# Optimization experiments

Hardware: AMD Instinct MI355X
Metric: run time of the kernel (lower is better)

## Reference

```python
import jax, jax.numpy as jnp
import numpy as np

_PADE_B = np.array([6.476475253248e+16, 3.238237626624e+16, 7771770303897600.0,
                    1187353796428800.0, 129060195264000.0, 10559470521600.0,
                    670442572800.0, 33522128640.0, 1323241920.0, 40840800.0,
                    960960.0, 16380.0, 182.0, 1.0])
_MAXNORM = 5.371920351148152
_MAX_SQUARINGS = 6  # randn 3x3 has Fro norm ~3 < maxnorm; 6 steps is ample headroom


def _expm(A):
    """Batched scaling-and-squaring Pade-13 matrix exponential. A: [N, d, d]."""
    b = _PADE_B.astype(A.dtype)
    d = A.shape[-1]
    ident = jnp.eye(d, dtype=A.dtype)
    fro = jnp.sqrt(jnp.sum(A * A, axis=(1, 2), keepdims=True))  # [N,1,1]
    n_sq = jnp.maximum(0.0, jnp.ceil(jnp.log2(fro / _MAXNORM)))
    Ascaled = A / (2.0 ** n_sq)
    n_sq_i = n_sq.reshape(-1).astype(jnp.int32)  # [N]

    A2 = Ascaled @ Ascaled
    A4 = A2 @ A2
    A6 = A4 @ A2
    U = Ascaled @ (A6 @ (b[13] * A6 + b[11] * A4 + b[9] * A2)
                   + b[7] * A6 + b[5] * A4 + b[3] * A2 + b[1] * ident)
    V = (A6 @ (b[12] * A6 + b[10] * A4 + b[8] * A2)
         + b[6] * A6 + b[4] * A4 + b[2] * A2 + b[0] * ident)
    P = U + V
    Q = -U + V
    R = jnp.linalg.solve(Q, P)  # torch.solve(P, Q): Q X = P

    def body(k, R):
        R2 = R @ R
        return jnp.where((k < n_sq_i)[:, None, None], R2, R)

    return jax.lax.fori_loop(0, _MAX_SQUARINGS, body, R, unroll=True)


def setup_inputs() -> dict:
    key = jax.random.key(0)
    k1, k2, k3 = jax.random.split(key, 3)
    bs, n, d = 65536, 24, 3
    return {
        "mean": jax.random.normal(k1, (bs, n, d), dtype=jnp.float32),
        "var": jax.random.normal(k2, (bs, n, d, d), dtype=jnp.float32),
        "gt": jax.random.normal(k3, (bs, n, d), dtype=jnp.float32),
    }


def reference(mean, var, gt):
    bs, n, d = mean.shape
    A = var.reshape(bs * n, d, d)
    E = _expm(A)                               # [bs*n, d, d]
    delta = (gt - mean).reshape(bs * n, d)     # [bs*n, d]
    quad = jnp.einsum('ni,nij,nj->n', delta, E, delta)
    dets = jnp.linalg.det(A)
    per = 0.5 * (quad + dets) / n              # [bs*n]
    loss = per.reshape(bs, n).sum(axis=1)      # [bs]
    return loss.mean()
```

## Files before the change

### kernel.cpp

```cpp
#include <hip/hip_runtime.h>

#define TPB 256

#define B0c  6.476475253248e+16f
#define B1c  3.238237626624e+16f
#define B2c  7.7717703038976e+15f
#define B3c  1.1873537964288e+15f
#define B4c  1.29060195264e+14f
#define B5c  1.05594705216e+13f
#define B6c  6.704425728e+11f
#define B7c  3.352212864e+10f
#define B8c  1.32324192e+9f
#define B9c  4.08408e+7f
#define B10c 9.6096e+5f
#define B11c 1.638e+4f
#define B12c 182.0f
#define B13c 1.0f

__device__ __forceinline__ float expm_loss_one(
    float a0, float a1, float a2, float a3, float a4, float a5,
    float a6, float a7, float a8, float d0, float d1, float d2) {
  const float detA = a0 * (a4 * a8 - a5 * a7)
                   - a1 * (a3 * a8 - a5 * a6)
                   + a2 * (a3 * a7 - a4 * a6);
  const float trA = a0 + a4 + a8;
  const float trA2 = fmaf(a0, a0, fmaf(a4, a4, a8 * a8))
                   + 2.0f * (fmaf(a1, a3, fmaf(a2, a6, a5 * a7)));
  float fro2 = fmaf(a0, a0, fmaf(a1, a1, a2 * a2));
  fro2 = fmaf(a3, a3, fmaf(a4, a4, fmaf(a5, a5, fro2)));
  fro2 = fmaf(a6, a6, fmaf(a7, a7, fmaf(a8, a8, fro2)));
  const float u0 = fmaf(a0, d0, fmaf(a1, d1, a2 * d2));
  const float u1 = fmaf(a3, d0, fmaf(a4, d1, a5 * d2));
  const float u2 = fmaf(a6, d0, fmaf(a7, d1, a8 * d2));
  const float v0 = fmaf(a0, d0, fmaf(a3, d1, a6 * d2));
  const float v1 = fmaf(a1, d0, fmaf(a4, d1, a7 * d2));
  const float v2 = fmaf(a2, d0, fmaf(a5, d1, a8 * d2));
  const float dAd  = fmaf(d0, u0, fmaf(d1, u1, d2 * u2));
  const float dA2d = fmaf(v0, u0, fmaf(v1, u1, v2 * u2));
  const float dd   = fmaf(d0, d0, fmaf(d1, d1, d2 * d2));

  const float nsqf = fmaxf(0.0f, ceilf(fmaf(0.5f, __log2f(fro2), -2.4253625f)));
  int nsq = (int)nsqf;
  nsq = nsq > 6 ? 6 : nsq;
  const float scl = exp2f(-nsqf);
  const float scl2 = scl * scl;

  const float t = scl * trA;
  const float trB2 = scl2 * trA2;
  const float m = 0.5f * fmaf(t, t, -trB2);
  const float dch = detA * scl2 * scl;

  const float x4p = fmaf(t, t, -m), x4q = fmaf(-t, m, dch), x4r = t * dch;
  const float x5p = fmaf(x4p, t, x4q), x5q = fmaf(-x4p, m, x4r), x5r = x4p * dch;
  const float x6p = fmaf(x5p, t, x5q), x6q = fmaf(-x5p, m, x5r), x6r = x5p * dch;

  const float w1p = fmaf(B11c, x4p, x6p) + B9c;
  const float w1q = fmaf(B11c, x4q, x6q);
  const float w1r = fmaf(B11c, x4r, x6r);
  const float s4a = x6p * w1p;
  const float s3a = fmaf(x6p, w1q, x6q * w1p);
  const float gp = fmaf(s4a, x4p, fmaf(s3a, t,   fmaf(x6p, w1r, fmaf(x6r, w1p, x6q * w1q))));
  const float gq = fmaf(s4a, x4q, fmaf(-s3a, m,  fmaf(x6q, w1r, x6r * w1q)));
  const float gr = fmaf(s4a, x4r, fmaf(s3a, dch, x6r * w1r));
  const float uep = fmaf(B7c, x6p, fmaf(B5c, x4p, gp)) + B3c;
  const float ueq = fmaf(B7c, x6q, fmaf(B5c, x4q, gq));
  const float uer = fmaf(B7c, x6r, fmaf(B5c, x4r, gr)) + B1c;
  const float up = fmaf(uep, t, ueq);
  const float uq = fmaf(-uep, m, uer);
  const float ur = uep * dch;

  const float w2p = fmaf(B12c, x6p, fmaf(B10c, x4p, B8c));
  const float w2q = fmaf(B12c, x6q, B10c * x4q);
  const float w2r = fmaf(B12c, x6r, B10c * x4r);
  const float s4b = x6p * w2p;
  const float s3b = fmaf(x6p, w2q, x6q * w2p);
  const float hp = fmaf(s4b, x4p, fmaf(s3b, t,   fmaf(x6p, w2r, fmaf(x6r, w2p, x6q * w2q))));
  const float hq = fmaf(s4b, x4q, fmaf(-s3b, m,  fmaf(x6q, w2r, x6r * w2q)));
  const float hr = fmaf(s4b, x4r, fmaf(s3b, dch, x6r * w2r));
  const float vp = fmaf(B6c, x6p, fmaf(B4c, x4p, hp)) + B2c;
  const float vq = fmaf(B6c, x6q, fmaf(B4c, x4q, hq));
  const float vr = fmaf(B6c, x6r, fmaf(B4c, x4r, hr)) + B0c;

  const float s = 1.0f / B0c;
  const float pp = (vp + up) * s, pq = (vq + uq) * s, pr = (vr + ur) * s;
  const float qp = (vp - up) * s, qq = (vq - uq) * s, qr = (vr - ur) * s;

  const float qpp = qp * qp, qpq2 = 2.0f * qp * qq;
  const float a2t = fmaf(qpp, x4p, fmaf(qpq2, t,   fmaf(2.0f * qp, qr, qq * qq)));
  const float b2t = fmaf(qpp, x4q, fmaf(-qpq2, m,  2.0f * qq * qr));
  const float c2t = fmaf(qpp, x4r, fmaf(qpq2, dch, qr * qr));
  const float tQ = fmaf(qp, trB2, fmaf(qq, t, 3.0f * qr));
  const float trQ2 = fmaf(a2t, trB2, fmaf(b2t, t, 3.0f * c2t));
  const float mQ = 0.5f * fmaf(tQ, tQ, -trQ2);
  const float detQ =
      qp * (fmaf(qp, fmaf(qp, dch * dch, fmaf(qq, m * dch, qr * fmaf(m, m, -2.0f * t * dch))),
                 fmaf(qq, fmaf(qq, t * dch, qr * fmaf(t, m, -3.0f * dch)),
                      qr * qr * fmaf(t, t, -2.0f * m))))
    + qq * fmaf(qq, fmaf(qq, dch, qr * m), qr * qr * t)
    + qr * qr * qr;
  float inv = __builtin_amdgcn_rcpf(detQ);
  inv = inv * (2.0f - detQ * inv);
  const float jp = fmaf(-tQ, qp, a2t);
  const float jq = fmaf(-tQ, qq, b2t);
  const float jr = fmaf(-tQ, qr, c2t) + mQ;

  const float s4 = pp * jp;
  const float s3 = fmaf(pp, jq, pq * jp);
  float rp = fmaf(s4, x4p, fmaf(s3, t,   fmaf(pp, jr, fmaf(pr, jp, pq * jq)))) * inv;
  float rq = fmaf(s4, x4q, fmaf(-s3, m,  fmaf(pq, jr, pr * jq))) * inv;
  float rr = fmaf(s4, x4r, fmaf(s3, dch, pr * jr)) * inv;

  for (int k = 0; k < nsq; ++k) {
    const float rp2 = rp * rp, rpq2 = 2.0f * rp * rq;
    const float nrp = fmaf(rp2, x4p, fmaf(rpq2, t,   fmaf(2.0f * rp, rr, rq * rq)));
    const float nrq = fmaf(rp2, x4q, fmaf(-rpq2, m,  2.0f * rq * rr));
    const float nrr = fmaf(rp2, x4r, fmaf(rpq2, dch, rr * rr));
    rp = nrp; rq = nrq; rr = nrr;
  }

  const float quad = fmaf(rp, scl2 * dA2d, fmaf(rq, scl * dAd, rr * dd));
  return 0.5f * (quad + detA);
}

__global__ __launch_bounds__(TPB) void expm_loss_kernel(
    const float* __restrict__ mean, const float* __restrict__ var,
    const float* __restrict__ gt, float* __restrict__ partials) {
  const int tid = threadIdx.x;
  const long long ti = (long long)blockIdx.x * TPB + tid;

  const float4* vp = (const float4*)var + ti * 9;
  const float4 w0 = vp[0], w1 = vp[1], w2 = vp[2], w3 = vp[3], w4 = vp[4],
               w5 = vp[5], w6 = vp[6], w7 = vp[7], w8 = vp[8];
  const float4* mp = (const float4*)mean + ti * 3;
  const float4* gp = (const float4*)gt + ti * 3;
  const float4 mw0 = mp[0], mw1 = mp[1], mw2 = mp[2];
  const float4 gw0 = gp[0], gw1 = gp[1], gw2 = gp[2];

  float val = expm_loss_one(w0.x, w0.y, w0.z, w0.w, w1.x, w1.y, w1.z, w1.w, w2.x,
                            gw0.x - mw0.x, gw0.y - mw0.y, gw0.z - mw0.z);
  val += expm_loss_one(w2.y, w2.z, w2.w, w3.x, w3.y, w3.z, w3.w, w4.x, w4.y,
                       gw0.w - mw0.w, gw1.x - mw1.x, gw1.y - mw1.y);
  val += expm_loss_one(w4.z, w4.w, w5.x, w5.y, w5.z, w5.w, w6.x, w6.y, w6.z,
                       gw1.z - mw1.z, gw1.w - mw1.w, gw2.x - mw2.x);
  val += expm_loss_one(w6.w, w7.x, w7.y, w7.z, w7.w, w8.x, w8.y, w8.z, w8.w,
                       gw2.y - mw2.y, gw2.z - mw2.z, gw2.w - mw2.w);

#pragma unroll
  for (int offx = 32; offx > 0; offx >>= 1) val += __shfl_down(val, offx, 64);
  __shared__ float wsum[TPB / 64];
  if ((tid & 63) == 0) wsum[tid >> 6] = val;
  __syncthreads();
  if (tid == 0) {
    float b = 0.f;
#pragma unroll
    for (int wi = 0; wi < TPB / 64; ++wi) b += wsum[wi];
    partials[blockIdx.x] = b;
  }
}

__global__ __launch_bounds__(256) void reduce_partials_kernel(
    const float* __restrict__ partials, int n, double inv_total,
    float* __restrict__ out) {
  double s = 0.0;
  for (int i = threadIdx.x; i < n; i += 256) s += (double)partials[i];
#pragma unroll
  for (int off = 32; off > 0; off >>= 1) s += __shfl_down(s, off, 64);
  __shared__ double ds[4];
  if ((threadIdx.x & 63) == 0) ds[threadIdx.x >> 6] = s;
  __syncthreads();
  if (threadIdx.x == 0)
    out[0] = (float)((ds[0] + ds[1] + ds[2] + ds[3]) * inv_total);
}

extern "C" void kernel_launch(void* const* d_in, const int* in_sizes, int n_in,
                              void* d_out, int out_size, void* d_ws, size_t ws_size,
                              hipStream_t stream) {
  const float* mean = (const float*)d_in[0];
  const float* var  = (const float*)d_in[1];
  const float* gt   = (const float*)d_in[2];
  const int nmat    = in_sizes[1] / 9;
  const int nblocks = nmat / (TPB * 4);
  float* partials   = (float*)d_ws;

  expm_loss_kernel<<<nblocks, TPB, 0, stream>>>(mean, var, gt, partials);
  reduce_partials_kernel<<<1, 256, 0, stream>>>(partials, nblocks,
                                                1.0 / (double)nmat,
                                                (float*)d_out);
}
```

Before: 23.81 us.

## Stage inputs through shared memory with one matrix per thread

```diff
diff --git a/kernel.cpp b/kernel.cpp
--- a/kernel.cpp
+++ b/kernel.cpp
@@ -125,25 +125,28 @@
 __global__ __launch_bounds__(TPB) void expm_loss_kernel(
     const float* __restrict__ mean, const float* __restrict__ var,
     const float* __restrict__ gt, float* __restrict__ partials) {
+  __shared__ float sA[TPB * 9];
+  __shared__ float sD[TPB * 3];
   const int tid = threadIdx.x;
-  const long long ti = (long long)blockIdx.x * TPB + tid;
+  const long long base = (long long)blockIdx.x * TPB;
 
-  const float4* vp = (const float4*)var + ti * 9;
-  const float4 w0 = vp[0], w1 = vp[1], w2 = vp[2], w3 = vp[3], w4 = vp[4],
-               w5 = vp[5], w6 = vp[6], w7 = vp[7], w8 = vp[8];
-  const float4* mp = (const float4*)mean + ti * 3;
-  const float4* gp = (const float4*)gt + ti * 3;
-  const float4 mw0 = mp[0], mw1 = mp[1], mw2 = mp[2];
-  const float4 gw0 = gp[0], gw1 = gp[1], gw2 = gp[2];
+  const float4* v4 = (const float4*)(var + base * 9);
+  float4* sA4 = (float4*)sA;
+  sA4[tid]       = v4[tid];
+  sA4[tid + 256] = v4[tid + 256];
+  if (tid < 64) sA4[tid + 512] = v4[tid + 512];
+  if (tid < 192) {
+    const float4 mw = ((const float4*)(mean + base * 3))[tid];
+    const float4 gw = ((const float4*)(gt + base * 3))[tid];
+    ((float4*)sD)[tid] = make_float4(gw.x - mw.x, gw.y - mw.y,
+                                     gw.z - mw.z, gw.w - mw.w);
+  }
+  __syncthreads();
 
-  float val = expm_loss_one(w0.x, w0.y, w0.z, w0.w, w1.x, w1.y, w1.z, w1.w, w2.x,
-                            gw0.x - mw0.x, gw0.y - mw0.y, gw0.z - mw0.z);
-  val += expm_loss_one(w2.y, w2.z, w2.w, w3.x, w3.y, w3.z, w3.w, w4.x, w4.y,
-                       gw0.w - mw0.w, gw1.x - mw1.x, gw1.y - mw1.y);
-  val += expm_loss_one(w4.z, w4.w, w5.x, w5.y, w5.z, w5.w, w6.x, w6.y, w6.z,
-                       gw1.z - mw1.z, gw1.w - mw1.w, gw2.x - mw2.x);
-  val += expm_loss_one(w6.w, w7.x, w7.y, w7.z, w7.w, w8.x, w8.y, w8.z, w8.w,
-                       gw2.y - mw2.y, gw2.z - mw2.z, gw2.w - mw2.w);
+  const float* a = sA + tid * 9;
+  const float* dp = sD + tid * 3;
+  float val = expm_loss_one(a[0], a[1], a[2], a[3], a[4], a[5], a[6], a[7], a[8],
+                            dp[0], dp[1], dp[2]);
 
 #pragma unroll
   for (int offx = 32; offx > 0; offx >>= 1) val += __shfl_down(val, offx, 64);
@@ -158,18 +161,23 @@
   }
 }
 
-__global__ __launch_bounds__(256) void reduce_partials_kernel(
+#define RTPB 1024
+__global__ __launch_bounds__(RTPB) void reduce_partials_kernel(
     const float* __restrict__ partials, int n, double inv_total,
     float* __restrict__ out) {
   double s = 0.0;
-  for (int i = threadIdx.x; i < n; i += 256) s += (double)partials[i];
+  for (int i = threadIdx.x; i < n; i += RTPB) s += (double)partials[i];
 #pragma unroll
   for (int off = 32; off > 0; off >>= 1) s += __shfl_down(s, off, 64);
-  __shared__ double ds[4];
+  __shared__ double ds[RTPB / 64];
   if ((threadIdx.x & 63) == 0) ds[threadIdx.x >> 6] = s;
   __syncthreads();
-  if (threadIdx.x == 0)
-    out[0] = (float)((ds[0] + ds[1] + ds[2] + ds[3]) * inv_total);
+  if (threadIdx.x == 0) {
+    double b = 0.0;
+#pragma unroll
+    for (int w = 0; w < RTPB / 64; ++w) b += ds[w];
+    out[0] = (float)(b * inv_total);
+  }
 }
 
 extern "C" void kernel_launch(void* const* d_in, const int* in_sizes, int n_in,
@@ -179,11 +187,11 @@
   const float* var  = (const float*)d_in[1];
   const float* gt   = (const float*)d_in[2];
   const int nmat    = in_sizes[1] / 9;
-  const int nblocks = nmat / (TPB * 4);
+  const int nblocks = nmat / TPB;
   float* partials   = (float*)d_ws;
 
   expm_loss_kernel<<<nblocks, TPB, 0, stream>>>(mean, var, gt, partials);
-  reduce_partials_kernel<<<1, 256, 0, stream>>>(partials, nblocks,
-                                                1.0 / (double)nmat,
-                                                (float*)d_out);
+  reduce_partials_kernel<<<1, RTPB, 0, stream>>>(partials, nblocks,
+                                                 1.0 / (double)nmat,
+                                                 (float*)d_out);
 }
```

Result: slower. 24.99 us (+4.9%).
